# Kernel tuning notes

Hardware: AMD Instinct MI355X
Metric: run time of the kernel (lower is better)

## Reference

```python
import jax, jax.numpy as jnp
import numpy as np

N = 100_000      # nodes
E = 1_600_000    # edges
IN, H, OUT = 128, 64, 32


def _gcn_edges(edge_index, n):
    """Add self-loops and compute symmetric GCN normalization (PyG gcn_norm)."""
    src, dst = edge_index[0], edge_index[1]
    loops = jnp.arange(n, dtype=src.dtype)
    src = jnp.concatenate([src, loops])
    dst = jnp.concatenate([dst, loops])
    deg = jax.ops.segment_sum(jnp.ones_like(dst, jnp.float32), dst, num_segments=n)
    dinv = jnp.where(deg > 0, jax.lax.rsqrt(deg), 0.0)
    norm = dinv[src] * dinv[dst]          # [E+N]
    return src, dst, norm


def _gcn_conv(x, src, dst, norm, W, b, n):
    h = x @ W.T                           # dense transform [n, out]
    msg = h[src] * norm[:, None]          # gather + scale per edge
    out = jax.ops.segment_sum(msg, dst, num_segments=n)  # scatter-add
    return out + b


def setup_inputs() -> dict:
    key = jax.random.key(0)
    k1, k2, k3, k4 = jax.random.split(key, 4)
    x = jax.random.normal(k1, (N, IN), dtype=jnp.float32)
    edge_index = jax.random.randint(k2, (2, E), 0, N, dtype=jnp.int32)
    # xavier_normal_: std = sqrt(2 / (fan_in + fan_out))
    W1 = jax.random.normal(k3, (H, IN), dtype=jnp.float32) * np.sqrt(2.0 / (IN + H))
    b1 = jnp.zeros((H,), dtype=jnp.float32)
    W2 = jax.random.normal(k4, (OUT, H), dtype=jnp.float32) * np.sqrt(2.0 / (H + OUT))
    b2 = jnp.zeros((OUT,), dtype=jnp.float32)
    return {"x": x, "edge_index": edge_index, "W1": W1, "b1": b1, "W2": W2, "b2": b2}


def reference(x, edge_index, W1, b1, W2, b2):
    n = x.shape[0]
    src, dst, norm = _gcn_edges(edge_index, n)
    h = _gcn_conv(x, src, dst, norm, W1, b1, n)
    h = jax.nn.relu(h)
    out = _gcn_conv(h, src, dst, norm, W2, b2, n)
    return out
```

## Files before the change

kernel.cpp:

```cpp
#include <hip/hip_runtime.h>

#define THREADS 256
#define G1 256
#define MAXNB 4096

using bf16x8 = __attribute__((ext_vector_type(8))) short;
using f32x4 = __attribute__((ext_vector_type(4))) float;

static __device__ __forceinline__ unsigned short f2bf(float f) {
  unsigned u = __float_as_uint(f);
  unsigned r = (u + 0x7fff + ((u >> 16) & 1)) >> 16;
  return (unsigned short)r;
}
static __device__ __forceinline__ float bflo(unsigned w) {
  return __uint_as_float(w << 16);
}
static __device__ __forceinline__ float bfhi(unsigned w) {
  return __uint_as_float(w & 0xffff0000u);
}
static __device__ __forceinline__ unsigned pk2(float a, float b) {
  return (unsigned)f2bf(a) | ((unsigned)f2bf(b) << 16);
}


__global__ void k_scan_chunk(const int* __restrict__ cnt, int* __restrict__ rp,
                             int* __restrict__ bsum, int m) {
  __shared__ int s[256];
  int b = blockIdx.x, t = threadIdx.x;
  int base = b * 1024 + t * 4;
  int v[4];
  int sum = 0;
#pragma unroll
  for (int k = 0; k < 4; ++k) {
    int i = base + k;
    v[k] = (i < m) ? cnt[i] : 0;
    sum += v[k];
  }
  s[t] = sum;
  __syncthreads();
  int mine = sum;
  for (int off = 1; off < 256; off <<= 1) {
    int y = (t >= off) ? s[t - off] : 0;
    __syncthreads();
    s[t] += y;
    __syncthreads();
  }
  int run = s[t] - mine;
  if (t == 255) bsum[b] = s[255];
#pragma unroll
  for (int k = 0; k < 4; ++k) {
    int i = base + k;
    if (i <= m) rp[i] = run;
    run += v[k];
  }
}

__global__ void k_scan_bsum(int* __restrict__ bsum, int nb) {
  __shared__ int s[256];
  int t = threadIdx.x;
  int v = (t < nb) ? bsum[t] : 0;
  s[t] = v;
  __syncthreads();
  for (int off = 1; off < 256; off <<= 1) {
    int y = (t >= off) ? s[t - off] : 0;
    __syncthreads();
    s[t] += y;
    __syncthreads();
  }
  if (t < nb) bsum[t] = s[t] - v;
}

__global__ void k_add(int* __restrict__ a, const int* __restrict__ bsum, int m) {
  int i = blockIdx.x * blockDim.x + threadIdx.x;
  if (i < m) a[i] += bsum[i >> 10];
}


__global__ void k_zrow(unsigned* __restrict__ h1b, unsigned* __restrict__ h2b, int n) {
  int t = threadIdx.x;
  if (t < 16) h1b[(size_t)n * 32 + t] = 0u;
  else if (t < 24) h2b[(size_t)n * 16 + (t - 16)] = 0u;
}


__launch_bounds__(256)
__global__ void k_pcount(const int* __restrict__ dst, int* __restrict__ C, int e,
                         int NB, int chunk) {
  __shared__ int h[MAXNB];
  int blk = blockIdx.x, t = threadIdx.x;
  for (int i = t; i < NB; i += 256) h[i] = 0;
  __syncthreads();
  int beg = blk * chunk;
  int stop = min(e, beg + chunk);
  for (int j = beg + t; j < stop; j += 256) atomicAdd(&h[dst[j] >> 7], 1);
  __syncthreads();
  for (int i = t; i < NB; i += 256) C[i * G1 + blk] = h[i];
}

__launch_bounds__(256)
__global__ void k_partition(const int* __restrict__ src, const int* __restrict__ dst,
                            const int* __restrict__ Cs, int* __restrict__ bpack, int e,
                            int NB, int chunk) {
  __shared__ int cur[MAXNB];
  int blk = blockIdx.x, t = threadIdx.x;
  for (int i = t; i < NB; i += 256) cur[i] = Cs[i * G1 + blk];
  __syncthreads();
  int beg = blk * chunk;
  int stop = min(e, beg + chunk);
  for (int j = beg + t; j < stop; j += 256) {
    int d = dst[j];
    int b = d >> 7;
    int pos = atomicAdd(&cur[b], 1);
    bpack[pos] = (src[j] << 7) | (d & 127);
  }
}

__launch_bounds__(256)
__global__ void k_bucket_csr(const int* __restrict__ bpack, const int* __restrict__ Cs,
                             int* __restrict__ rp, float* __restrict__ dinv,
                             int* __restrict__ csr_src, int n, int e, int NB) {
  __shared__ int cl[128];
  __shared__ int cur[128];
  int blk = blockIdx.x, t = threadIdx.x;
  int base = Cs[blk * G1];
  int end = (blk == NB - 1) ? e : Cs[(blk + 1) * G1];
  if (t < 128) cl[t] = 0;
  __syncthreads();
  for (int j = base + t; j < end; j += 256) atomicAdd(&cl[bpack[j] & 127], 1);
  __syncthreads();
  int own = (t < 128) ? cl[t] : 0;
  for (int off = 1; off < 128; off <<= 1) {
    int y = (t >= off && t < 128) ? cl[t - off] : 0;
    __syncthreads();
    if (t < 128) cl[t] += y;
    __syncthreads();
  }
  if (t < 128) {
    int excl = cl[t] - own;
    int v = (blk << 7) + t;
    if (v < n) {
      rp[v] = base + excl;
      dinv[v] = rsqrtf((float)own + 1.0f);
    }
    cur[t] = base + excl;
  }
  __syncthreads();
  for (int j = base + t; j < end; j += 256) {
    int p = bpack[j];
    int pos = atomicAdd(&cur[p & 127], 1);
    csr_src[pos] = p >> 7;
  }
  if (blk == 0 && t == 0) rp[n] = e;
}


__launch_bounds__(256)
__global__ void k_gemm1(const float* __restrict__ x, const float* __restrict__ W1,
                        const float* __restrict__ dinv, unsigned short* __restrict__ h1b,
                        int n) {
  __shared__ uint4 sXb[64 * 16];
  __shared__ uint4 sWb[64 * 16];
  __shared__ __align__(16) unsigned short sOut[64 * 64];
  int t = threadIdx.x;
  const float4* x4 = (const float4*)x;
  const float4* W14 = (const float4*)W1;
  int rbase = blockIdx.x * 64;
#pragma unroll
  for (int p = 0; p < 4; ++p) {
    int q = t + 256 * p;
    int r = q >> 4, s = q & 15;
    int gr = rbase + r;
    float4 v0 = make_float4(0.f, 0.f, 0.f, 0.f), v1 = v0;
    if (gr < n) {
      v0 = x4[(size_t)gr * 32 + s * 2];
      v1 = x4[(size_t)gr * 32 + s * 2 + 1];
    }
    uint4 pk;
    pk.x = pk2(v0.x, v0.y);
    pk.y = pk2(v0.z, v0.w);
    pk.z = pk2(v1.x, v1.y);
    pk.w = pk2(v1.z, v1.w);
    sXb[r * 16 + (s ^ (r & 15))] = pk;
  }
#pragma unroll
  for (int p = 0; p < 4; ++p) {
    int q = t + 256 * p;
    int c = q >> 4, s = q & 15;
    float4 v0 = W14[c * 32 + s * 2];
    float4 v1 = W14[c * 32 + s * 2 + 1];
    uint4 pk;
    pk.x = pk2(v0.x, v0.y);
    pk.y = pk2(v0.z, v0.w);
    pk.z = pk2(v1.x, v1.y);
    pk.w = pk2(v1.z, v1.w);
    sWb[c * 16 + (s ^ (c & 15))] = pk;
  }
  __syncthreads();
  int lane = t & 63;
  int w = t >> 6;
  int l16 = lane & 15, quad = lane >> 4;
  int arow = w * 16 + l16;
  f32x4 acc0 = {0.f, 0.f, 0.f, 0.f};
  f32x4 acc1 = {0.f, 0.f, 0.f, 0.f};
  f32x4 acc2 = {0.f, 0.f, 0.f, 0.f};
  f32x4 acc3 = {0.f, 0.f, 0.f, 0.f};
#pragma unroll
  for (int kc = 0; kc < 4; ++kc) {
    int slot = kc * 4 + quad;
    uint4 ua = sXb[arow * 16 + (slot ^ (arow & 15))];
    bf16x8 a = *(bf16x8*)&ua;
    uint4 ub0 = sWb[(0 + l16) * 16 + (slot ^ l16)];
    uint4 ub1 = sWb[(16 + l16) * 16 + (slot ^ l16)];
    uint4 ub2 = sWb[(32 + l16) * 16 + (slot ^ l16)];
    uint4 ub3 = sWb[(48 + l16) * 16 + (slot ^ l16)];
    acc0 = __builtin_amdgcn_mfma_f32_16x16x32_bf16(a, *(bf16x8*)&ub0, acc0, 0, 0, 0);
    acc1 = __builtin_amdgcn_mfma_f32_16x16x32_bf16(a, *(bf16x8*)&ub1, acc1, 0, 0, 0);
    acc2 = __builtin_amdgcn_mfma_f32_16x16x32_bf16(a, *(bf16x8*)&ub2, acc2, 0, 0, 0);
    acc3 = __builtin_amdgcn_mfma_f32_16x16x32_bf16(a, *(bf16x8*)&ub3, acc3, 0, 0, 0);
  }
  float dvr[4];
#pragma unroll
  for (int r = 0; r < 4; ++r) {
    int grow = rbase + w * 16 + quad * 4 + r;
    dvr[r] = (grow < n) ? dinv[grow] : 0.f;
  }
#pragma unroll
  for (int r = 0; r < 4; ++r) {
    int rl = w * 16 + quad * 4 + r;
    sOut[rl * 64 + 0 + l16] = f2bf(acc0[r] * dvr[r]);
    sOut[rl * 64 + 16 + l16] = f2bf(acc1[r] * dvr[r]);
    sOut[rl * 64 + 32 + l16] = f2bf(acc2[r] * dvr[r]);
    sOut[rl * 64 + 48 + l16] = f2bf(acc3[r] * dvr[r]);
  }
  __syncthreads();
#pragma unroll
  for (int p = 0; p < 2; ++p) {
    int q = t + 256 * p;
    int r = q >> 3, s = q & 7;
    int gr = rbase + r;
    if (gr < n)
      *(uint4*)&h1b[(size_t)gr * 64 + s * 8] = *(uint4*)&sOut[r * 64 + s * 8];
  }
}


__launch_bounds__(256)
__global__ void k_agg1(const unsigned* __restrict__ h1p, const float* __restrict__ dinv,
                       const int* __restrict__ rp, const int* __restrict__ csr_src,
                       float* __restrict__ agg1, int n) {
  int gid = blockIdx.x * 256 + threadIdx.x;
  int v = gid >> 5, f2 = gid & 31;
  if (v >= n) return;
  int beg = rp[v], end = rp[v + 1];
  unsigned w0 = h1p[(size_t)v * 32 + f2];
  float ax0 = bflo(w0), ay0 = bfhi(w0);
  float ax1 = 0.f, ay1 = 0.f, ax2 = 0.f, ay2 = 0.f, ax3 = 0.f, ay3 = 0.f;
  float ax4 = 0.f, ay4 = 0.f, ax5 = 0.f, ay5 = 0.f, ax6 = 0.f, ay6 = 0.f;
  float ax7 = 0.f, ay7 = 0.f;
  for (int j = beg; j < end; j += 8) {
    int s0 = csr_src[j];
    int s1 = csr_src[j + 1];
    int s2 = csr_src[j + 2];
    int s3 = csr_src[j + 3];
    int s4 = csr_src[j + 4];
    int s5 = csr_src[j + 5];
    int s6 = csr_src[j + 6];
    int s7 = csr_src[j + 7];
    s1 = (j + 1 < end) ? s1 : n;
    s2 = (j + 2 < end) ? s2 : n;
    s3 = (j + 3 < end) ? s3 : n;
    s4 = (j + 4 < end) ? s4 : n;
    s5 = (j + 5 < end) ? s5 : n;
    s6 = (j + 6 < end) ? s6 : n;
    s7 = (j + 7 < end) ? s7 : n;
    unsigned g0 = h1p[(size_t)s0 * 32 + f2];
    unsigned g1 = h1p[(size_t)s1 * 32 + f2];
    unsigned g2 = h1p[(size_t)s2 * 32 + f2];
    unsigned g3 = h1p[(size_t)s3 * 32 + f2];
    unsigned g4 = h1p[(size_t)s4 * 32 + f2];
    unsigned g5 = h1p[(size_t)s5 * 32 + f2];
    unsigned g6 = h1p[(size_t)s6 * 32 + f2];
    unsigned g7 = h1p[(size_t)s7 * 32 + f2];
    ax0 += bflo(g0); ay0 += bfhi(g0);
    ax1 += bflo(g1); ay1 += bfhi(g1);
    ax2 += bflo(g2); ay2 += bfhi(g2);
    ax3 += bflo(g3); ay3 += bfhi(g3);
    ax4 += bflo(g4); ay4 += bfhi(g4);
    ax5 += bflo(g5); ay5 += bfhi(g5);
    ax6 += bflo(g6); ay6 += bfhi(g6);
    ax7 += bflo(g7); ay7 += bfhi(g7);
  }
  float dv = dinv[v];
  float sx = ((ax0 + ax1) + (ax2 + ax3)) + ((ax4 + ax5) + (ax6 + ax7));
  float sy = ((ay0 + ay1) + (ay2 + ay3)) + ((ay4 + ay5) + (ay6 + ay7));
  *(float2*)&agg1[(size_t)v * 64 + f2 * 2] = make_float2(dv * sx, dv * sy);
}


__launch_bounds__(256)
__global__ void k_gemm2(const float* __restrict__ agg1, const float* __restrict__ b1,
                        const float* __restrict__ W2, const float* __restrict__ dinv,
                        unsigned short* __restrict__ h2b, int n) {
  __shared__ float4 sW4[32 * 16];
  __shared__ float4 sX4[256 * 8];
  int t = threadIdx.x;
  const float4* W24 = (const float4*)W2;
  const float4* a4 = (const float4*)agg1;
  const float4* b14 = (const float4*)b1;
#pragma unroll
  for (int p = 0; p < 2; ++p) {
    int q = t + 256 * p;
    int c = q >> 4, m = q & 15;
    sW4[c * 16 + (m ^ ((c >> 3) & 7))] = W24[c * 16 + m];
  }
  int cg = t & 3;
  int rg = t >> 2;
  int rbase = blockIdx.x * 256;
  int r0 = rbase + rg * 4;
  float acc[4][8] = {{0.f}};
  for (int ci = 0; ci < 2; ++ci) {
    __syncthreads();
#pragma unroll
    for (int p = 0; p < 8; ++p) {
      int q = t + 256 * p;
      int r = q >> 3, s = q & 7;
      int gr = rbase + r;
      float4 v = make_float4(0.f, 0.f, 0.f, 0.f);
      if (gr < n) {
        float4 a = a4[(size_t)gr * 16 + ci * 8 + s];
        float4 b = b14[ci * 8 + s];
        v = make_float4(fmaxf(a.x + b.x, 0.f), fmaxf(a.y + b.y, 0.f),
                        fmaxf(a.z + b.z, 0.f), fmaxf(a.w + b.w, 0.f));
      }
      sX4[r * 8 + (s ^ ((r >> 2) & 7))] = v;
    }
    __syncthreads();
#pragma unroll
    for (int k4 = 0; k4 < 8; ++k4) {
      int kf4 = ci * 8 + k4;
      float4 xv[4], wv[8];
#pragma unroll
      for (int i = 0; i < 4; ++i)
        xv[i] = sX4[(rg * 4 + i) * 8 + (k4 ^ (rg & 7))];
#pragma unroll
      for (int j = 0; j < 8; ++j)
        wv[j] = sW4[(cg * 8 + j) * 16 + (kf4 ^ cg)];
#pragma unroll
      for (int i = 0; i < 4; ++i)
#pragma unroll
        for (int j = 0; j < 8; ++j) {
          acc[i][j] = fmaf(xv[i].x, wv[j].x, acc[i][j]);
          acc[i][j] = fmaf(xv[i].y, wv[j].y, acc[i][j]);
          acc[i][j] = fmaf(xv[i].z, wv[j].z, acc[i][j]);
          acc[i][j] = fmaf(xv[i].w, wv[j].w, acc[i][j]);
        }
    }
  }
#pragma unroll
  for (int i = 0; i < 4; ++i) {
    int gr = r0 + i;
    if (gr < n) {
      float dv = dinv[gr];
      union {
        unsigned short us[8];
        uint4 u4;
      } pk;
#pragma unroll
      for (int j = 0; j < 8; ++j) pk.us[j] = f2bf(acc[i][j] * dv);
      *(uint4*)&h2b[(size_t)gr * 32 + cg * 8] = pk.u4;
    }
  }
}


__launch_bounds__(256)
__global__ void k_agg2(const unsigned* __restrict__ h2p, const float* __restrict__ dinv,
                       const int* __restrict__ rp, const int* __restrict__ csr_src,
                       const float* __restrict__ b2, float* __restrict__ out, int n) {
  int gid = blockIdx.x * 256 + threadIdx.x;
  int v = gid >> 4, f2 = gid & 15;
  if (v >= n) return;
  int beg = rp[v], end = rp[v + 1];
  unsigned w0 = h2p[(size_t)v * 16 + f2];
  float ax0 = bflo(w0), ay0 = bfhi(w0);
  float ax1 = 0.f, ay1 = 0.f, ax2 = 0.f, ay2 = 0.f, ax3 = 0.f, ay3 = 0.f;
  float ax4 = 0.f, ay4 = 0.f, ax5 = 0.f, ay5 = 0.f, ax6 = 0.f, ay6 = 0.f;
  float ax7 = 0.f, ay7 = 0.f;
  for (int j = beg; j < end; j += 8) {
    int s0 = csr_src[j];
    int s1 = csr_src[j + 1];
    int s2 = csr_src[j + 2];
    int s3 = csr_src[j + 3];
    int s4 = csr_src[j + 4];
    int s5 = csr_src[j + 5];
    int s6 = csr_src[j + 6];
    int s7 = csr_src[j + 7];
    s1 = (j + 1 < end) ? s1 : n;
    s2 = (j + 2 < end) ? s2 : n;
    s3 = (j + 3 < end) ? s3 : n;
    s4 = (j + 4 < end) ? s4 : n;
    s5 = (j + 5 < end) ? s5 : n;
    s6 = (j + 6 < end) ? s6 : n;
    s7 = (j + 7 < end) ? s7 : n;
    unsigned g0 = h2p[(size_t)s0 * 16 + f2];
    unsigned g1 = h2p[(size_t)s1 * 16 + f2];
    unsigned g2 = h2p[(size_t)s2 * 16 + f2];
    unsigned g3 = h2p[(size_t)s3 * 16 + f2];
    unsigned g4 = h2p[(size_t)s4 * 16 + f2];
    unsigned g5 = h2p[(size_t)s5 * 16 + f2];
    unsigned g6 = h2p[(size_t)s6 * 16 + f2];
    unsigned g7 = h2p[(size_t)s7 * 16 + f2];
    ax0 += bflo(g0); ay0 += bfhi(g0);
    ax1 += bflo(g1); ay1 += bfhi(g1);
    ax2 += bflo(g2); ay2 += bfhi(g2);
    ax3 += bflo(g3); ay3 += bfhi(g3);
    ax4 += bflo(g4); ay4 += bfhi(g4);
    ax5 += bflo(g5); ay5 += bfhi(g5);
    ax6 += bflo(g6); ay6 += bfhi(g6);
    ax7 += bflo(g7); ay7 += bfhi(g7);
  }
  float dv = dinv[v];
  float sx = ((ax0 + ax1) + (ax2 + ax3)) + ((ax4 + ax5) + (ax6 + ax7));
  float sy = ((ay0 + ay1) + (ay2 + ay3)) + ((ay4 + ay5) + (ay6 + ay7));
  float2 bv = *(const float2*)&b2[f2 * 2];
  *(float2*)&out[(size_t)v * 32 + f2 * 2] =
      make_float2(fmaf(dv, sx, bv.x), fmaf(dv, sy, bv.y));
}


extern "C" void kernel_launch(void* const* d_in, const int* in_sizes, int n_in,
                              void* d_out, int out_size, void* d_ws, size_t ws_size,
                              hipStream_t stream) {
  const float* x = (const float*)d_in[0];
  const int* ei = (const int*)d_in[1];
  const float* W1 = (const float*)d_in[2];
  const float* b1 = (const float*)d_in[3];
  const float* W2 = (const float*)d_in[4];
  const float* b2 = (const float*)d_in[5];
  float* out = (float*)d_out;

  const int n = in_sizes[0] / 128;
  const int e = in_sizes[1] / 2;
  const int* src = ei;
  const int* dst = ei + e;

  const int NB = (n + 127) >> 7;
  const int m = NB * G1;
  const int chunk = (e + G1 - 1) / G1;
  const int NC = (m + 1 + 1023) / 1024;

  char* base = (char*)d_ws;
  size_t off = 0;
  auto alloc = [&](size_t bytes) {
    char* p = base + off;
    off = (off + bytes + 255) & ~(size_t)255;
    return p;
  };
  int* C = (int*)alloc((size_t)m * 4);
  int* Cs = (int*)alloc((size_t)(m + 1) * 4);
  int* bsum = (int*)alloc(1024 * 4);
  int* bpack = (int*)alloc((size_t)e * 4);
  int* rp = (int*)alloc((size_t)(n + 1) * 4);
  int* csr_src = (int*)alloc((size_t)(e + 8) * 4);
  float* dinv = (float*)alloc((size_t)n * 4);
  unsigned short* h1b = (unsigned short*)alloc((size_t)(n + 1) * 64 * 2);
  float* agg1 = (float*)alloc((size_t)n * 64 * 4);
  unsigned short* h2b = (unsigned short*)alloc((size_t)(n + 1) * 32 * 2);

  k_zrow<<<1, 64, 0, stream>>>((unsigned*)h1b, (unsigned*)h2b, n);
  k_pcount<<<G1, 256, 0, stream>>>(dst, C, e, NB, chunk);
  k_scan_chunk<<<NC, 256, 0, stream>>>(C, Cs, bsum, m);
  k_scan_bsum<<<1, 256, 0, stream>>>(bsum, NC);
  k_add<<<(m + 255) / 256, 256, 0, stream>>>(Cs, bsum, m);
  k_partition<<<G1, 256, 0, stream>>>(src, dst, Cs, bpack, e, NB, chunk);
  k_bucket_csr<<<NB, 256, 0, stream>>>(bpack, Cs, rp, dinv, csr_src, n, e, NB);

  k_gemm1<<<(n + 63) / 64, 256, 0, stream>>>(x, W1, dinv, h1b, n);
  {
    long long total = (long long)n * 32;
    k_agg1<<<(int)((total + 255) / 256), 256, 0, stream>>>((const unsigned*)h1b, dinv,
                                                           rp, csr_src, agg1, n);
  }

  k_gemm2<<<(n + 255) / 256, 256, 0, stream>>>(agg1, b1, W2, dinv, h2b, n);
  {
    long long total = (long long)n * 16;
    k_agg2<<<(int)((total + 255) / 256), 256, 0, stream>>>((const unsigned*)h2b, dinv,
                                                           rp, csr_src, b2, out, n);
  }
}
```

Before: 225.1 us.

## Store agg1 in bf16 and use MFMA for the second GEMM

The first aggregation now writes its output as packed bf16 instead of fp32, halving that intermediate's write and read traffic. The second GEMM is rewritten to apply bias and ReLU, convert the activations and W2 to bf16 in LDS, and run 16x16x32 bf16 MFMA instructions instead of scalar fp32 FMAs. Its block size drops to 64 rows and output is staged through LDS for coalesced stores. Precision is reduced, since activations and weights are rounded to bf16 before the second transform.

```diff
diff --git a/kernel.cpp b/kernel.cpp
--- a/kernel.cpp
+++ b/kernel.cpp
@@ -247,7 +247,7 @@
 __launch_bounds__(256)
 __global__ void k_agg1(const unsigned* __restrict__ h1p, const float* __restrict__ dinv,
                        const int* __restrict__ rp, const int* __restrict__ csr_src,
-                       float* __restrict__ agg1, int n) {
+                       unsigned* __restrict__ agg1b, int n) {
   int gid = blockIdx.x * 256 + threadIdx.x;
   int v = gid >> 5, f2 = gid & 31;
   if (v >= n) return;
@@ -293,82 +293,84 @@
   float dv = dinv[v];
   float sx = ((ax0 + ax1) + (ax2 + ax3)) + ((ax4 + ax5) + (ax6 + ax7));
   float sy = ((ay0 + ay1) + (ay2 + ay3)) + ((ay4 + ay5) + (ay6 + ay7));
-  *(float2*)&agg1[(size_t)v * 64 + f2 * 2] = make_float2(dv * sx, dv * sy);
-}
-
-
-__launch_bounds__(256)
-__global__ void k_gemm2(const float* __restrict__ agg1, const float* __restrict__ b1,
+  agg1b[(size_t)v * 32 + f2] = pk2(dv * sx, dv * sy);
+}
+
+
+__launch_bounds__(256)
+__global__ void k_gemm2(const unsigned* __restrict__ agg1b, const float* __restrict__ b1,
                         const float* __restrict__ W2, const float* __restrict__ dinv,
                         unsigned short* __restrict__ h2b, int n) {
-  __shared__ float4 sW4[32 * 16];
-  __shared__ float4 sX4[256 * 8];
+  __shared__ uint4 sXb[64 * 8];
+  __shared__ uint4 sWb[32 * 8];
+  __shared__ __align__(16) unsigned short sOut[64 * 32];
   int t = threadIdx.x;
+  int rbase = blockIdx.x * 64;
+  const uint4* a4 = (const uint4*)agg1b;
+  const float4* b14 = (const float4*)b1;
   const float4* W24 = (const float4*)W2;
-  const float4* a4 = (const float4*)agg1;
-  const float4* b14 = (const float4*)b1;
 #pragma unroll
   for (int p = 0; p < 2; ++p) {
     int q = t + 256 * p;
-    int c = q >> 4, m = q & 15;
-    sW4[c * 16 + (m ^ ((c >> 3) & 7))] = W24[c * 16 + m];
-  }
-  int cg = t & 3;
-  int rg = t >> 2;
-  int rbase = blockIdx.x * 256;
-  int r0 = rbase + rg * 4;
-  float acc[4][8] = {{0.f}};
-  for (int ci = 0; ci < 2; ++ci) {
-    __syncthreads();
-#pragma unroll
-    for (int p = 0; p < 8; ++p) {
-      int q = t + 256 * p;
-      int r = q >> 3, s = q & 7;
-      int gr = rbase + r;
-      float4 v = make_float4(0.f, 0.f, 0.f, 0.f);
-      if (gr < n) {
-        float4 a = a4[(size_t)gr * 16 + ci * 8 + s];
-        float4 b = b14[ci * 8 + s];
-        v = make_float4(fmaxf(a.x + b.x, 0.f), fmaxf(a.y + b.y, 0.f),
-                        fmaxf(a.z + b.z, 0.f), fmaxf(a.w + b.w, 0.f));
-      }
-      sX4[r * 8 + (s ^ ((r >> 2) & 7))] = v;
+    int r = q >> 3, s = q & 7;
+    int gr = rbase + r;
+    uint4 o = make_uint4(0u, 0u, 0u, 0u);
+    if (gr < n) {
+      uint4 a = a4[(size_t)gr * 8 + s];
+      float4 blo = b14[s * 2], bhi = b14[s * 2 + 1];
+      o.x = pk2(fmaxf(bflo(a.x) + blo.x, 0.f), fmaxf(bfhi(a.x) + blo.y, 0.f));
+      o.y = pk2(fmaxf(bflo(a.y) + blo.z, 0.f), fmaxf(bfhi(a.y) + blo.w, 0.f));
+      o.z = pk2(fmaxf(bflo(a.z) + bhi.x, 0.f), fmaxf(bfhi(a.z) + bhi.y, 0.f));
+      o.w = pk2(fmaxf(bflo(a.w) + bhi.z, 0.f), fmaxf(bfhi(a.w) + bhi.w, 0.f));
     }
-    __syncthreads();
-#pragma unroll
-    for (int k4 = 0; k4 < 8; ++k4) {
-      int kf4 = ci * 8 + k4;
-      float4 xv[4], wv[8];
-#pragma unroll
-      for (int i = 0; i < 4; ++i)
-        xv[i] = sX4[(rg * 4 + i) * 8 + (k4 ^ (rg & 7))];
-#pragma unroll
-      for (int j = 0; j < 8; ++j)
-        wv[j] = sW4[(cg * 8 + j) * 16 + (kf4 ^ cg)];
-#pragma unroll
-      for (int i = 0; i < 4; ++i)
-#pragma unroll
-        for (int j = 0; j < 8; ++j) {
-          acc[i][j] = fmaf(xv[i].x, wv[j].x, acc[i][j]);
-          acc[i][j] = fmaf(xv[i].y, wv[j].y, acc[i][j]);
-          acc[i][j] = fmaf(xv[i].z, wv[j].z, acc[i][j]);
-          acc[i][j] = fmaf(xv[i].w, wv[j].w, acc[i][j]);
-        }
-    }
-  }
-#pragma unroll
-  for (int i = 0; i < 4; ++i) {
-    int gr = r0 + i;
-    if (gr < n) {
-      float dv = dinv[gr];
-      union {
-        unsigned short us[8];
-        uint4 u4;
-      } pk;
-#pragma unroll
-      for (int j = 0; j < 8; ++j) pk.us[j] = f2bf(acc[i][j] * dv);
-      *(uint4*)&h2b[(size_t)gr * 32 + cg * 8] = pk.u4;
-    }
+    sXb[r * 8 + (s ^ (r & 7))] = o;
+  }
+  {
+    int c = t >> 3, s = t & 7;
+    float4 v0 = W24[c * 16 + s * 2];
+    float4 v1 = W24[c * 16 + s * 2 + 1];
+    uint4 pk;
+    pk.x = pk2(v0.x, v0.y);
+    pk.y = pk2(v0.z, v0.w);
+    pk.z = pk2(v1.x, v1.y);
+    pk.w = pk2(v1.z, v1.w);
+    sWb[c * 8 + (s ^ (c & 7))] = pk;
+  }
+  __syncthreads();
+  int lane = t & 63;
+  int w = t >> 6;
+  int l16 = lane & 15, quad = lane >> 4;
+  int arow = w * 16 + l16;
+  f32x4 acc0 = {0.f, 0.f, 0.f, 0.f};
+  f32x4 acc1 = {0.f, 0.f, 0.f, 0.f};
+#pragma unroll
+  for (int kc = 0; kc < 2; ++kc) {
+    int slot = kc * 4 + quad;
+    uint4 ua = sXb[arow * 8 + (slot ^ (arow & 7))];
+    bf16x8 a = *(bf16x8*)&ua;
+    uint4 ub0 = sWb[l16 * 8 + (slot ^ (l16 & 7))];
+    uint4 ub1 = sWb[(16 + l16) * 8 + (slot ^ (l16 & 7))];
+    acc0 = __builtin_amdgcn_mfma_f32_16x16x32_bf16(a, *(bf16x8*)&ub0, acc0, 0, 0, 0);
+    acc1 = __builtin_amdgcn_mfma_f32_16x16x32_bf16(a, *(bf16x8*)&ub1, acc1, 0, 0, 0);
+  }
+  float dvr[4];
+#pragma unroll
+  for (int r = 0; r < 4; ++r) {
+    int grow = rbase + w * 16 + quad * 4 + r;
+    dvr[r] = (grow < n) ? dinv[grow] : 0.f;
+  }
+#pragma unroll
+  for (int r = 0; r < 4; ++r) {
+    int rl = w * 16 + quad * 4 + r;
+    sOut[rl * 32 + l16] = f2bf(acc0[r] * dvr[r]);
+    sOut[rl * 32 + 16 + l16] = f2bf(acc1[r] * dvr[r]);
+  }
+  __syncthreads();
+  {
+    int r = t >> 2, s = t & 3;
+    int gr = rbase + r;
+    if (gr < n)
+      *(uint4*)&h2b[(size_t)gr * 32 + s * 8] = *(uint4*)&sOut[r * 32 + s * 8];
   }
 }
 
@@ -464,7 +466,7 @@
   int* csr_src = (int*)alloc((size_t)(e + 8) * 4);
   float* dinv = (float*)alloc((size_t)n * 4);
   unsigned short* h1b = (unsigned short*)alloc((size_t)(n + 1) * 64 * 2);
-  float* agg1 = (float*)alloc((size_t)n * 64 * 4);
+  unsigned* agg1b = (unsigned*)alloc((size_t)n * 64 * 2);
   unsigned short* h2b = (unsigned short*)alloc((size_t)(n + 1) * 32 * 2);
 
   k_zrow<<<1, 64, 0, stream>>>((unsigned*)h1b, (unsigned*)h2b, n);
@@ -479,10 +481,10 @@
   {
     long long total = (long long)n * 32;
     k_agg1<<<(int)((total + 255) / 256), 256, 0, stream>>>((const unsigned*)h1b, dinv,
-                                                           rp, csr_src, agg1, n);
-  }
-
-  k_gemm2<<<(n + 255) / 256, 256, 0, stream>>>(agg1, b1, W2, dinv, h2b, n);
+                                                           rp, csr_src, agg1b, n);
+  }
+
+  k_gemm2<<<(n + 63) / 64, 256, 0, stream>>>(agg1b, b1, W2, dinv, h2b, n);
   {
     long long total = (long long)n * 16;
     k_agg2<<<(int)((total + 255) / 256), 256, 0, stream>>>((const unsigned*)h2b, dinv,
```

Result: faster. 216.5 us (-3.8%).
